# Optimization experiments

Measured on AMD Instinct MI355X. Metric: run time of the kernel, lower is better.

The kernel has to match this reference:

```python
import jax, jax.numpy as jnp
import numpy as np

EPS = 1e-08


def setup_inputs() -> dict:
    key = jax.random.key(0)
    k1, k2, k3 = jax.random.split(key, 3)
    N = 4000000
    x = jax.random.normal(k1, (N, 3), dtype=jnp.float32)
    x_gt = jax.random.normal(k2, (N, 3), dtype=jnp.float32)
    weights = jax.random.uniform(k3, (N,), dtype=jnp.float32)
    return {"x": x, "x_gt": x_gt, "weights": weights}


def reference(x, x_gt, weights):
    # weights: [N] -> [N, 1]
    w = weights[:, None]
    weight_sum = w.sum() + EPS
    mu = (w * x).sum(axis=0, keepdims=True) / weight_sum        # [1, 3]
    mu_gt = (w * x_gt).sum(axis=0, keepdims=True) / weight_sum  # [1, 3]
    x_c = x - mu
    x_gt_c = x_gt - mu_gt
    sw = jnp.sqrt(w)
    # H = (sqrt(w)*x_c)^T @ (sqrt(w)*x_gt_c)  -> [3, 3]
    H = jnp.einsum('ni,nj->ij', sw * x_c, sw * x_gt_c)
    U, S, Vt = jnp.linalg.svd(H)
    R = U @ Vt  # == U @ V.T with V = Vt.T
    det_R = jnp.linalg.det(R)
    # Reflection fix: R = U @ diag(1,1,d) @ Vt with d = -1 if det < 0
    d = jnp.where(det_R < 0, -1.0, 1.0).astype(R.dtype)
    F = jnp.array([1.0, 1.0, 0.0], dtype=R.dtype) + jnp.array([0.0, 0.0, 1.0], dtype=R.dtype) * d
    R = (U * F[None, :]) @ Vt
    # x_aligned = (R @ x_gt_c^T)^T + mu = x_gt_c @ R^T + mu
    x_aligned = x_gt_c @ R.T + mu
    return jax.lax.stop_gradient(x_aligned)
```

## Files before the change

### kernel.cpp

```cpp
#include <hip/hip_runtime.h>
#include <math.h>

typedef float    f32x4 __attribute__((ext_vector_type(4)));
typedef _Float16 f16x4 __attribute__((ext_vector_type(4)));

#define BLK 256

__device__ __forceinline__ void accum4(
    float a[16], f32x4 xa, f32x4 xb, f32x4 xc,
    f32x4 ga, f32x4 gb, f32x4 gc, f32x4 wv)
{
    float px[4] = {xa.x, xa.w, xb.z, xc.y};
    float py[4] = {xa.y, xb.x, xb.w, xc.z};
    float pz[4] = {xa.z, xb.y, xc.x, xc.w};
    float qx[4] = {ga.x, ga.w, gb.z, gc.y};
    float qy[4] = {ga.y, gb.x, gb.w, gc.z};
    float qz[4] = {ga.z, gb.y, gc.x, gc.w};
    float wt[4] = {wv.x, wv.y, wv.z, wv.w};
#pragma unroll
    for (int k = 0; k < 4; ++k) {
        float wk = wt[k];
        float wpx = wk * px[k], wpy = wk * py[k], wpz = wk * pz[k];
        a[0] += wk;
        a[1] += wpx;         a[2] += wpy;         a[3] += wpz;
        a[4] += wk * qx[k];  a[5] += wk * qy[k];  a[6] += wk * qz[k];
        a[7]  += wpx * qx[k]; a[8]  += wpx * qy[k]; a[9]  += wpx * qz[k];
        a[10] += wpy * qx[k]; a[11] += wpy * qy[k]; a[12] += wpy * qz[k];
        a[13] += wpz * qx[k]; a[14] += wpz * qy[k]; a[15] += wpz * qz[k];
    }
}

__global__ __launch_bounds__(BLK) void wra_reduce(
    const float* __restrict__ x, const float* __restrict__ g,
    const float* __restrict__ w, float* __restrict__ partials,
    f16x4* __restrict__ g16, int n4, int n)
{
    float a[16];
#pragma unroll
    for (int i = 0; i < 16; ++i) a[i] = 0.f;

    const f32x4* __restrict__ x4 = (const f32x4*)x;
    const f32x4* __restrict__ g4 = (const f32x4*)g;
    const f32x4* __restrict__ w4 = (const f32x4*)w;

    int tid = blockIdx.x * blockDim.x + threadIdx.x;
    int stride = gridDim.x * blockDim.x;

    int i = tid;
    for (; i + stride < n4; i += 2 * stride) {
        int j = i + stride;
        f32x4 xa0 = __builtin_nontemporal_load(&x4[3*i+0]);
        f32x4 xb0 = __builtin_nontemporal_load(&x4[3*i+1]);
        f32x4 xc0 = __builtin_nontemporal_load(&x4[3*i+2]);
        f32x4 ga0 = g4[3*i+0];
        f32x4 gb0 = g4[3*i+1];
        f32x4 gc0 = g4[3*i+2];
        f32x4 wv0 = __builtin_nontemporal_load(&w4[i]);
        f32x4 xa1 = __builtin_nontemporal_load(&x4[3*j+0]);
        f32x4 xb1 = __builtin_nontemporal_load(&x4[3*j+1]);
        f32x4 xc1 = __builtin_nontemporal_load(&x4[3*j+2]);
        f32x4 ga1 = g4[3*j+0];
        f32x4 gb1 = g4[3*j+1];
        f32x4 gc1 = g4[3*j+2];
        f32x4 wv1 = __builtin_nontemporal_load(&w4[j]);
        if (g16) {
            g16[3*i+0] = __builtin_convertvector(ga0, f16x4);
            g16[3*i+1] = __builtin_convertvector(gb0, f16x4);
            g16[3*i+2] = __builtin_convertvector(gc0, f16x4);
            g16[3*j+0] = __builtin_convertvector(ga1, f16x4);
            g16[3*j+1] = __builtin_convertvector(gb1, f16x4);
            g16[3*j+2] = __builtin_convertvector(gc1, f16x4);
        }
        accum4(a, xa0, xb0, xc0, ga0, gb0, gc0, wv0);
        accum4(a, xa1, xb1, xc1, ga1, gb1, gc1, wv1);
    }
    for (; i < n4; i += stride) {
        f32x4 xa = __builtin_nontemporal_load(&x4[3*i+0]);
        f32x4 xb = __builtin_nontemporal_load(&x4[3*i+1]);
        f32x4 xc = __builtin_nontemporal_load(&x4[3*i+2]);
        f32x4 ga = g4[3*i+0];
        f32x4 gb = g4[3*i+1];
        f32x4 gc = g4[3*i+2];
        f32x4 wv = __builtin_nontemporal_load(&w4[i]);
        if (g16) {
            g16[3*i+0] = __builtin_convertvector(ga, f16x4);
            g16[3*i+1] = __builtin_convertvector(gb, f16x4);
            g16[3*i+2] = __builtin_convertvector(gc, f16x4);
        }
        accum4(a, xa, xb, xc, ga, gb, gc, wv);
    }

    if (blockIdx.x == 0 && threadIdx.x == 0) {
        for (int r = n4 * 4; r < n; ++r) {
            float wk = w[r];
            float X = x[3*r], Y = x[3*r+1], Z = x[3*r+2];
            float Gx = g[3*r], Gy = g[3*r+1], Gz = g[3*r+2];
            float wpx = wk * X, wpy = wk * Y, wpz = wk * Z;
            a[0] += wk;
            a[1] += wpx;      a[2] += wpy;      a[3] += wpz;
            a[4] += wk * Gx;  a[5] += wk * Gy;  a[6] += wk * Gz;
            a[7]  += wpx * Gx; a[8]  += wpx * Gy; a[9]  += wpx * Gz;
            a[10] += wpy * Gx; a[11] += wpy * Gy; a[12] += wpy * Gz;
            a[13] += wpz * Gx; a[14] += wpz * Gy; a[15] += wpz * Gz;
        }
    }

#pragma unroll
    for (int i2 = 0; i2 < 16; ++i2) {
        float v = a[i2];
        for (int off = 32; off > 0; off >>= 1) v += __shfl_down(v, off, 64);
        a[i2] = v;
    }
    __shared__ float red[4][16];
    int lane = threadIdx.x & 63;
    int wid  = threadIdx.x >> 6;
    if (lane == 0) {
#pragma unroll
        for (int i2 = 0; i2 < 16; ++i2) red[wid][i2] = a[i2];
    }
    __syncthreads();
    if (threadIdx.x < 16) {
        float s = red[0][threadIdx.x] + red[1][threadIdx.x]
                + red[2][threadIdx.x] + red[3][threadIdx.x];
        partials[blockIdx.x * 16 + threadIdx.x] = s;
    }
}

__global__ __launch_bounds__(64) void wra_solve(
    const float* __restrict__ partials, int nb, float* __restrict__ rt)
{
    int lane = threadIdx.x;
    double acc[16];
#pragma unroll
    for (int i = 0; i < 16; ++i) acc[i] = 0.0;
    for (int b = lane; b < nb; b += 64) {
#pragma unroll
        for (int i = 0; i < 16; ++i) acc[i] += (double)partials[b * 16 + i];
    }
#pragma unroll
    for (int i = 0; i < 16; ++i) {
        double v = acc[i];
        for (int off = 32; off > 0; off >>= 1) v += __shfl_down(v, off, 64);
        acc[i] = v;
    }
    if (lane != 0) return;

    double Sw = acc[0];
    double Sx[3] = {acc[1], acc[2], acc[3]};
    double Sg[3] = {acc[4], acc[5], acc[6]};
    double Hr[3][3];
    for (int i = 0; i < 3; ++i)
        for (int j = 0; j < 3; ++j) Hr[i][j] = acc[7 + i * 3 + j];

    double W = Sw + 1e-8;
    double mu[3], mg[3];
    for (int i = 0; i < 3; ++i) { mu[i] = Sx[i] / W; mg[i] = Sg[i] / W; }

    double H[3][3];
    for (int i = 0; i < 3; ++i)
        for (int j = 0; j < 3; ++j)
            H[i][j] = Hr[i][j] - mu[i] * Sg[j] - mg[j] * Sx[i] + mu[i] * mg[j] * Sw;

    double A[3][3];
    for (int i = 0; i < 3; ++i)
        for (int j = 0; j < 3; ++j) {
            double s = 0.0;
            for (int k = 0; k < 3; ++k) s += H[k][i] * H[k][j];
            A[i][j] = s;
        }

    double V[3][3] = {{1,0,0},{0,1,0},{0,0,1}};
    const int pr[3] = {0, 0, 1}, qr[3] = {1, 2, 2};
    for (int sweep = 0; sweep < 10; ++sweep) {
        for (int r = 0; r < 3; ++r) {
            int p = pr[r], q = qr[r];
            double apq = A[p][q];
            if (fabs(apq) < 1e-30) continue;
            double tau = (A[q][q] - A[p][p]) / (2.0 * apq);
            double t = (tau >= 0 ? 1.0 : -1.0) / (fabs(tau) + sqrt(1.0 + tau * tau));
            double c = 1.0 / sqrt(1.0 + t * t), s = t * c;
            for (int k = 0; k < 3; ++k) {
                double akp = A[k][p], akq = A[k][q];
                A[k][p] = c * akp - s * akq;
                A[k][q] = s * akp + c * akq;
            }
            for (int k = 0; k < 3; ++k) {
                double apk = A[p][k], aqk = A[q][k];
                A[p][k] = c * apk - s * aqk;
                A[q][k] = s * apk + c * aqk;
            }
            for (int k = 0; k < 3; ++k) {
                double vkp = V[k][p], vkq = V[k][q];
                V[k][p] = c * vkp - s * vkq;
                V[k][q] = s * vkp + c * vkq;
            }
        }
    }
    double lam[3] = {A[0][0], A[1][1], A[2][2]};

    int idx[3] = {0, 1, 2};
    if (lam[idx[0]] < lam[idx[1]]) { int t = idx[0]; idx[0] = idx[1]; idx[1] = t; }
    if (lam[idx[1]] < lam[idx[2]]) { int t = idx[1]; idx[1] = idx[2]; idx[2] = t; }
    if (lam[idx[0]] < lam[idx[1]]) { int t = idx[0]; idx[0] = idx[1]; idx[1] = t; }

    double Vs[3][3], U[3][3];
    for (int k = 0; k < 3; ++k) {
        int c0 = idx[k];
        double l = lam[c0] > 1e-30 ? lam[c0] : 1e-30;
        double inv = 1.0 / sqrt(l);
        for (int i = 0; i < 3; ++i) Vs[i][k] = V[i][c0];
        for (int i = 0; i < 3; ++i) {
            double s = 0.0;
            for (int j = 0; j < 3; ++j) s += H[i][j] * Vs[j][k];
            U[i][k] = s * inv;
        }
    }

    double detH = H[0][0] * (H[1][1] * H[2][2] - H[1][2] * H[2][1])
                - H[0][1] * (H[1][0] * H[2][2] - H[1][2] * H[2][0])
                + H[0][2] * (H[1][0] * H[2][1] - H[1][1] * H[2][0]);
    double d = (detH < 0.0) ? -1.0 : 1.0;

    double R[3][3];
    for (int i = 0; i < 3; ++i)
        for (int j = 0; j < 3; ++j)
            R[i][j] = U[i][0] * Vs[j][0] + U[i][1] * Vs[j][1] + d * U[i][2] * Vs[j][2];

    double tv[3];
    for (int i = 0; i < 3; ++i)
        tv[i] = mu[i] - (R[i][0] * mg[0] + R[i][1] * mg[1] + R[i][2] * mg[2]);

    for (int i = 0; i < 3; ++i)
        for (int j = 0; j < 3; ++j) rt[i * 3 + j] = (float)R[i][j];
    for (int i = 0; i < 3; ++i) rt[9 + i] = (float)tv[i];
}

__global__ __launch_bounds__(BLK) void wra_apply_h(
    const f16x4* __restrict__ g16, const float* __restrict__ g,
    const float* __restrict__ rt, float* __restrict__ out,
    int n4, int n, int ntiles)
{
    __shared__ f16x4 ibuf[768];
    __shared__ f32x4 obuf[768];

    float R00 = rt[0], R01 = rt[1], R02 = rt[2];
    float R10 = rt[3], R11 = rt[4], R12 = rt[5];
    float R20 = rt[6], R21 = rt[7], R22 = rt[8];
    float t0 = rt[9], t1 = rt[10], t2 = rt[11];

    f32x4* __restrict__ o4 = (f32x4*)out;

    const int tid = threadIdx.x;
    const int totc = 3 * n4;

    for (int t = blockIdx.x; t < ntiles; t += gridDim.x) {
        const int cb = t * 768;
#pragma unroll
        for (int k = 0; k < 3; ++k) {
            int c = cb + tid + 256 * k;
            if (c < totc) ibuf[tid + 256 * k] = g16[c];
        }
        __syncthreads();

        f32x4 ga = __builtin_convertvector(ibuf[3 * tid + 0], f32x4);
        f32x4 gb = __builtin_convertvector(ibuf[3 * tid + 1], f32x4);
        f32x4 gc = __builtin_convertvector(ibuf[3 * tid + 2], f32x4);
        float qx0 = ga.x, qy0 = ga.y, qz0 = ga.z;
        float qx1 = ga.w, qy1 = gb.x, qz1 = gb.y;
        float qx2 = gb.z, qy2 = gb.w, qz2 = gc.x;
        float qx3 = gc.y, qy3 = gc.z, qz3 = gc.w;

        f32x4 r0, r1, r2;
        r0.x = R00*qx0 + R01*qy0 + R02*qz0 + t0;
        r0.y = R10*qx0 + R11*qy0 + R12*qz0 + t1;
        r0.z = R20*qx0 + R21*qy0 + R22*qz0 + t2;
        r0.w = R00*qx1 + R01*qy1 + R02*qz1 + t0;
        r1.x = R10*qx1 + R11*qy1 + R12*qz1 + t1;
        r1.y = R20*qx1 + R21*qy1 + R22*qz1 + t2;
        r1.z = R00*qx2 + R01*qy2 + R02*qz2 + t0;
        r1.w = R10*qx2 + R11*qy2 + R12*qz2 + t1;
        r2.x = R20*qx2 + R21*qy2 + R22*qz2 + t2;
        r2.y = R00*qx3 + R01*qy3 + R02*qz3 + t0;
        r2.z = R10*qx3 + R11*qy3 + R12*qz3 + t1;
        r2.w = R20*qx3 + R21*qy3 + R22*qz3 + t2;

        obuf[3 * tid + 0] = r0;
        obuf[3 * tid + 1] = r1;
        obuf[3 * tid + 2] = r2;
        __syncthreads();

#pragma unroll
        for (int k = 0; k < 3; ++k) {
            int c = cb + tid + 256 * k;
            if (c < totc) o4[c] = obuf[tid + 256 * k];
        }
        __syncthreads();
    }

    int gtid = blockIdx.x * blockDim.x + threadIdx.x;
    int gstr = gridDim.x * blockDim.x;
    for (int r = n4 * 4 + gtid; r < n; r += gstr) {
        float Gx = g[3*r], Gy = g[3*r+1], Gz = g[3*r+2];
        out[3*r+0] = R00*Gx + R01*Gy + R02*Gz + t0;
        out[3*r+1] = R10*Gx + R11*Gy + R12*Gz + t1;
        out[3*r+2] = R20*Gx + R21*Gy + R22*Gz + t2;
    }
}

__global__ __launch_bounds__(BLK) void wra_apply_f(
    const float* __restrict__ g, const float* __restrict__ rt,
    float* __restrict__ out, int n4, int n, int ntiles)
{
    __shared__ f32x4 buf[768];

    float R00 = rt[0], R01 = rt[1], R02 = rt[2];
    float R10 = rt[3], R11 = rt[4], R12 = rt[5];
    float R20 = rt[6], R21 = rt[7], R22 = rt[8];
    float t0 = rt[9], t1 = rt[10], t2 = rt[11];

    const f32x4* __restrict__ g4 = (const f32x4*)g;
    f32x4* __restrict__ o4 = (f32x4*)out;

    const int tid = threadIdx.x;
    const int totc = 3 * n4;

    for (int t = blockIdx.x; t < ntiles; t += gridDim.x) {
        const int cb = t * 768;
#pragma unroll
        for (int k = 0; k < 3; ++k) {
            int c = cb + tid + 256 * k;
            if (c < totc) buf[tid + 256 * k] = g4[c];
        }
        __syncthreads();

        f32x4 ga = buf[3 * tid + 0], gb = buf[3 * tid + 1], gc = buf[3 * tid + 2];
        float qx0 = ga.x, qy0 = ga.y, qz0 = ga.z;
        float qx1 = ga.w, qy1 = gb.x, qz1 = gb.y;
        float qx2 = gb.z, qy2 = gb.w, qz2 = gc.x;
        float qx3 = gc.y, qy3 = gc.z, qz3 = gc.w;

        f32x4 r0, r1, r2;
        r0.x = R00*qx0 + R01*qy0 + R02*qz0 + t0;
        r0.y = R10*qx0 + R11*qy0 + R12*qz0 + t1;
        r0.z = R20*qx0 + R21*qy0 + R22*qz0 + t2;
        r0.w = R00*qx1 + R01*qy1 + R02*qz1 + t0;
        r1.x = R10*qx1 + R11*qy1 + R12*qz1 + t1;
        r1.y = R20*qx1 + R21*qy1 + R22*qz1 + t2;
        r1.z = R00*qx2 + R01*qy2 + R02*qz2 + t0;
        r1.w = R10*qx2 + R11*qy2 + R12*qz2 + t1;
        r2.x = R20*qx2 + R21*qy2 + R22*qz2 + t2;
        r2.y = R00*qx3 + R01*qy3 + R02*qz3 + t0;
        r2.z = R10*qx3 + R11*qy3 + R12*qz3 + t1;
        r2.w = R20*qx3 + R21*qy3 + R22*qz3 + t2;

        buf[3 * tid + 0] = r0;
        buf[3 * tid + 1] = r1;
        buf[3 * tid + 2] = r2;
        __syncthreads();

#pragma unroll
        for (int k = 0; k < 3; ++k) {
            int c = cb + tid + 256 * k;
            if (c < totc) o4[c] = buf[tid + 256 * k];
        }
        __syncthreads();
    }

    int gtid = blockIdx.x * blockDim.x + threadIdx.x;
    int gstr = gridDim.x * blockDim.x;
    for (int r = n4 * 4 + gtid; r < n; r += gstr) {
        float Gx = g[3*r], Gy = g[3*r+1], Gz = g[3*r+2];
        out[3*r+0] = R00*Gx + R01*Gy + R02*Gz + t0;
        out[3*r+1] = R10*Gx + R11*Gy + R12*Gz + t1;
        out[3*r+2] = R20*Gx + R21*Gy + R22*Gz + t2;
    }
}

extern "C" void kernel_launch(void* const* d_in, const int* in_sizes, int n_in,
                              void* d_out, int out_size, void* d_ws, size_t ws_size,
                              hipStream_t stream)
{
    const float* x = (const float*)d_in[0];
    const float* g = (const float*)d_in[1];
    const float* w = (const float*)d_in[2];
    float* out = (float*)d_out;

    int n = in_sizes[2];
    int n4 = n / 4;
    int ntiles = (n4 + 255) / 256;
    if (ntiles < 1) ntiles = 1;

    int nbr = 2048;
    int need = (n4 + BLK - 1) / BLK;
    if (need < 1) need = 1;
    if (nbr > need) nbr = need;
    int maxnb = (int)((ws_size / sizeof(float) - 12) / 16);
    if (nbr > maxnb) nbr = maxnb;
    if (nbr < 1) nbr = 1;

    float* partials = (float*)d_ws;
    float* rt = partials + (size_t)nbr * 16;

    size_t base = ((size_t)nbr * 16 + 12) * sizeof(float);
    size_t g16off = (base + 255) & ~(size_t)255;
    size_t g16bytes = (size_t)3 * (size_t)n4 * sizeof(f16x4);
    bool use16 = (n4 > 0) && (ws_size >= g16off + g16bytes);
    f16x4* g16 = use16 ? (f16x4*)((char*)d_ws + g16off) : (f16x4*)nullptr;

    wra_reduce<<<nbr, BLK, 0, stream>>>(x, g, w, partials, g16, n4, n);
    wra_solve<<<1, 64, 0, stream>>>(partials, nbr, rt);

    int nba = ntiles < 2048 ? ntiles : 2048;
    if (use16)
        wra_apply_h<<<nba, BLK, 0, stream>>>(g16, g, rt, out, n4, n, ntiles);
    else
        wra_apply_f<<<nba, BLK, 0, stream>>>(g, rt, out, n4, n, ntiles);
}
```

Before: 59.77 us.

## Stage reduce-kernel loads through LDS for fully coalesced tile reads

The reduction kernel now walks 256-point tiles per block. Each thread loads consecutive float4 chunks of x and x_gt into shared memory, so global reads are fully coalesced, and then reads back its own 3-vector group from LDS. This replaces the per-thread strided 48-byte loads, which produced poorly coalesced accesses. The grid shrinks from 2048 to 1024 blocks and the nontemporal hints are dropped. In exchange there are two barriers per tile and extra LDS traffic, with less load-level parallelism per thread.

```diff
diff --git a/kernel.cpp b/kernel.cpp
--- a/kernel.cpp
+++ b/kernel.cpp
@@ -5,36 +5,15 @@
 typedef _Float16 f16x4 __attribute__((ext_vector_type(4)));
 
 #define BLK 256
-
-__device__ __forceinline__ void accum4(
-    float a[16], f32x4 xa, f32x4 xb, f32x4 xc,
-    f32x4 ga, f32x4 gb, f32x4 gc, f32x4 wv)
-{
-    float px[4] = {xa.x, xa.w, xb.z, xc.y};
-    float py[4] = {xa.y, xb.x, xb.w, xc.z};
-    float pz[4] = {xa.z, xb.y, xc.x, xc.w};
-    float qx[4] = {ga.x, ga.w, gb.z, gc.y};
-    float qy[4] = {ga.y, gb.x, gb.w, gc.z};
-    float qz[4] = {ga.z, gb.y, gc.x, gc.w};
-    float wt[4] = {wv.x, wv.y, wv.z, wv.w};
-#pragma unroll
-    for (int k = 0; k < 4; ++k) {
-        float wk = wt[k];
-        float wpx = wk * px[k], wpy = wk * py[k], wpz = wk * pz[k];
-        a[0] += wk;
-        a[1] += wpx;         a[2] += wpy;         a[3] += wpz;
-        a[4] += wk * qx[k];  a[5] += wk * qy[k];  a[6] += wk * qz[k];
-        a[7]  += wpx * qx[k]; a[8]  += wpx * qy[k]; a[9]  += wpx * qz[k];
-        a[10] += wpy * qx[k]; a[11] += wpy * qy[k]; a[12] += wpy * qz[k];
-        a[13] += wpz * qx[k]; a[14] += wpz * qy[k]; a[15] += wpz * qz[k];
-    }
-}
 
 __global__ __launch_bounds__(BLK) void wra_reduce(
     const float* __restrict__ x, const float* __restrict__ g,
     const float* __restrict__ w, float* __restrict__ partials,
-    f16x4* __restrict__ g16, int n4, int n)
-{
+    f16x4* __restrict__ g16, int n4, int n, int ntiles)
+{
+    __shared__ f32x4 xs[768];
+    __shared__ f32x4 gs[768];
+
     float a[16];
 #pragma unroll
     for (int i = 0; i < 16; ++i) a[i] = 0.f;
@@ -43,54 +22,50 @@
     const f32x4* __restrict__ g4 = (const f32x4*)g;
     const f32x4* __restrict__ w4 = (const f32x4*)w;
 
-    int tid = blockIdx.x * blockDim.x + threadIdx.x;
-    int stride = gridDim.x * blockDim.x;
-
-    int i = tid;
-    for (; i + stride < n4; i += 2 * stride) {
-        int j = i + stride;
-        f32x4 xa0 = __builtin_nontemporal_load(&x4[3*i+0]);
-        f32x4 xb0 = __builtin_nontemporal_load(&x4[3*i+1]);
-        f32x4 xc0 = __builtin_nontemporal_load(&x4[3*i+2]);
-        f32x4 ga0 = g4[3*i+0];
-        f32x4 gb0 = g4[3*i+1];
-        f32x4 gc0 = g4[3*i+2];
-        f32x4 wv0 = __builtin_nontemporal_load(&w4[i]);
-        f32x4 xa1 = __builtin_nontemporal_load(&x4[3*j+0]);
-        f32x4 xb1 = __builtin_nontemporal_load(&x4[3*j+1]);
-        f32x4 xc1 = __builtin_nontemporal_load(&x4[3*j+2]);
-        f32x4 ga1 = g4[3*j+0];
-        f32x4 gb1 = g4[3*j+1];
-        f32x4 gc1 = g4[3*j+2];
-        f32x4 wv1 = __builtin_nontemporal_load(&w4[j]);
-        if (g16) {
-            g16[3*i+0] = __builtin_convertvector(ga0, f16x4);
-            g16[3*i+1] = __builtin_convertvector(gb0, f16x4);
-            g16[3*i+2] = __builtin_convertvector(gc0, f16x4);
-            g16[3*j+0] = __builtin_convertvector(ga1, f16x4);
-            g16[3*j+1] = __builtin_convertvector(gb1, f16x4);
-            g16[3*j+2] = __builtin_convertvector(gc1, f16x4);
-        }
-        accum4(a, xa0, xb0, xc0, ga0, gb0, gc0, wv0);
-        accum4(a, xa1, xb1, xc1, ga1, gb1, gc1, wv1);
-    }
-    for (; i < n4; i += stride) {
-        f32x4 xa = __builtin_nontemporal_load(&x4[3*i+0]);
-        f32x4 xb = __builtin_nontemporal_load(&x4[3*i+1]);
-        f32x4 xc = __builtin_nontemporal_load(&x4[3*i+2]);
-        f32x4 ga = g4[3*i+0];
-        f32x4 gb = g4[3*i+1];
-        f32x4 gc = g4[3*i+2];
-        f32x4 wv = __builtin_nontemporal_load(&w4[i]);
-        if (g16) {
-            g16[3*i+0] = __builtin_convertvector(ga, f16x4);
-            g16[3*i+1] = __builtin_convertvector(gb, f16x4);
-            g16[3*i+2] = __builtin_convertvector(gc, f16x4);
-        }
-        accum4(a, xa, xb, xc, ga, gb, gc, wv);
-    }
-
-    if (blockIdx.x == 0 && threadIdx.x == 0) {
+    const int tid = threadIdx.x;
+    const int totc = 3 * n4;
+    const f32x4 z4 = {0.f, 0.f, 0.f, 0.f};
+
+    for (int t = blockIdx.x; t < ntiles; t += gridDim.x) {
+        const int cb = t * 768;
+#pragma unroll
+        for (int k = 0; k < 3; ++k) {
+            int c = cb + tid + 256 * k;
+            f32x4 xv = z4, gv = z4;
+            if (c < totc) { xv = x4[c]; gv = g4[c]; }
+            xs[tid + 256 * k] = xv;
+            gs[tid + 256 * k] = gv;
+            if (g16 && c < totc) g16[c] = __builtin_convertvector(gv, f16x4);
+        }
+        int wc = t * 256 + tid;
+        f32x4 wv = (wc < n4) ? w4[wc] : z4;
+        __syncthreads();
+
+        f32x4 xa = xs[3 * tid + 0], xb = xs[3 * tid + 1], xc = xs[3 * tid + 2];
+        f32x4 ga = gs[3 * tid + 0], gb = gs[3 * tid + 1], gc = gs[3 * tid + 2];
+
+        float px[4] = {xa.x, xa.w, xb.z, xc.y};
+        float py[4] = {xa.y, xb.x, xb.w, xc.z};
+        float pz[4] = {xa.z, xb.y, xc.x, xc.w};
+        float qx[4] = {ga.x, ga.w, gb.z, gc.y};
+        float qy[4] = {ga.y, gb.x, gb.w, gc.z};
+        float qz[4] = {ga.z, gb.y, gc.x, gc.w};
+        float wt[4] = {wv.x, wv.y, wv.z, wv.w};
+#pragma unroll
+        for (int k = 0; k < 4; ++k) {
+            float wk = wt[k];
+            float wpx = wk * px[k], wpy = wk * py[k], wpz = wk * pz[k];
+            a[0] += wk;
+            a[1] += wpx;         a[2] += wpy;         a[3] += wpz;
+            a[4] += wk * qx[k];  a[5] += wk * qy[k];  a[6] += wk * qz[k];
+            a[7]  += wpx * qx[k]; a[8]  += wpx * qy[k]; a[9]  += wpx * qz[k];
+            a[10] += wpy * qx[k]; a[11] += wpy * qy[k]; a[12] += wpy * qz[k];
+            a[13] += wpz * qx[k]; a[14] += wpz * qy[k]; a[15] += wpz * qz[k];
+        }
+        __syncthreads();
+    }
+
+    if (blockIdx.x == 0 && tid == 0) {
         for (int r = n4 * 4; r < n; ++r) {
             float wk = w[r];
             float X = x[3*r], Y = x[3*r+1], Z = x[3*r+2];
@@ -106,23 +81,22 @@
     }
 
 #pragma unroll
-    for (int i2 = 0; i2 < 16; ++i2) {
-        float v = a[i2];
+    for (int i = 0; i < 16; ++i) {
+        float v = a[i];
         for (int off = 32; off > 0; off >>= 1) v += __shfl_down(v, off, 64);
-        a[i2] = v;
+        a[i] = v;
     }
     __shared__ float red[4][16];
-    int lane = threadIdx.x & 63;
-    int wid  = threadIdx.x >> 6;
+    int lane = tid & 63;
+    int wid  = tid >> 6;
     if (lane == 0) {
 #pragma unroll
-        for (int i2 = 0; i2 < 16; ++i2) red[wid][i2] = a[i2];
+        for (int i = 0; i < 16; ++i) red[wid][i] = a[i];
     }
     __syncthreads();
-    if (threadIdx.x < 16) {
-        float s = red[0][threadIdx.x] + red[1][threadIdx.x]
-                + red[2][threadIdx.x] + red[3][threadIdx.x];
-        partials[blockIdx.x * 16 + threadIdx.x] = s;
+    if (tid < 16) {
+        float s = red[0][tid] + red[1][tid] + red[2][tid] + red[3][tid];
+        partials[blockIdx.x * 16 + tid] = s;
     }
 }
 
@@ -390,12 +364,10 @@
     int ntiles = (n4 + 255) / 256;
     if (ntiles < 1) ntiles = 1;
 
-    int nbr = 2048;
-    int need = (n4 + BLK - 1) / BLK;
-    if (need < 1) need = 1;
-    if (nbr > need) nbr = need;
+    int nbr = 1024;
     int maxnb = (int)((ws_size / sizeof(float) - 12) / 16);
     if (nbr > maxnb) nbr = maxnb;
+    if (nbr > ntiles) nbr = ntiles;
     if (nbr < 1) nbr = 1;
 
     float* partials = (float*)d_ws;
@@ -407,7 +379,7 @@
     bool use16 = (n4 > 0) && (ws_size >= g16off + g16bytes);
     f16x4* g16 = use16 ? (f16x4*)((char*)d_ws + g16off) : (f16x4*)nullptr;
 
-    wra_reduce<<<nbr, BLK, 0, stream>>>(x, g, w, partials, g16, n4, n);
+    wra_reduce<<<nbr, BLK, 0, stream>>>(x, g, w, partials, g16, n4, n, ntiles);
     wra_solve<<<1, 64, 0, stream>>>(partials, nbr, rt);
 
     int nba = ntiles < 2048 ? ntiles : 2048;
```

New measurement: 53.68 us, median of 2. 1.11x faster.
